# Performance work log

Hardware: AMD Instinct MI355X
Metric: run time of the kernel (lower is better)

Reference implementation:

```python
import jax, jax.numpy as jnp
import numpy as np

EMB_DIM = 512
QKV_DIM = 512
NUM_HEADS = 8
HEAD_DIM = QKV_DIM // NUM_HEADS  # 64
BATCH = 4
SEQLEN = 2048


def _gaussian_orthogonal_random_matrix(rng, nb_rows, nb_cols):
    # Matches torch gaussian_orthogonal_random_matrix with scaling=0.
    blocks = []
    n_full = nb_rows // nb_cols
    for _ in range(n_full):
        q, _ = np.linalg.qr(rng.standard_normal((nb_cols, nb_cols)))
        blocks.append(q.T)
    rem = nb_rows - n_full * nb_cols
    if rem > 0:
        q, _ = np.linalg.qr(rng.standard_normal((nb_cols, nb_cols)))
        blocks.append(q.T[:rem])
    mat = np.concatenate(blocks, axis=0)
    mult = np.linalg.norm(rng.standard_normal((nb_rows, nb_cols)), axis=1)
    return (mult[:, None] * mat).astype(np.float32)


def setup_inputs() -> dict:
    key = jax.random.key(0)
    ks = jax.random.split(key, 9)
    s = 0.02
    inp = {
        'x': jax.random.normal(ks[0], (BATCH, SEQLEN, EMB_DIM), jnp.float32),
        'Wq': jax.random.normal(ks[1], (EMB_DIM, QKV_DIM), jnp.float32) * s,
        'bq': jnp.zeros((QKV_DIM,), jnp.float32),
        'Wk': jax.random.normal(ks[2], (EMB_DIM, QKV_DIM), jnp.float32) * s,
        'bk': jnp.zeros((QKV_DIM,), jnp.float32),
        'Wv': jax.random.normal(ks[3], (EMB_DIM, QKV_DIM), jnp.float32) * s,
        'bv': jnp.zeros((QKV_DIM,), jnp.float32),
        'Wo': jax.random.normal(ks[4], (QKV_DIM, EMB_DIM), jnp.float32) * s,
        'bo': jnp.zeros((EMB_DIM,), jnp.float32),
        'proj': jnp.asarray(_gaussian_orthogonal_random_matrix(
            np.random.default_rng(0), QKV_DIM, HEAD_DIM)),  # (m=qkv_dim, head_dim)
    }
    return inp


def _split_heads(x):
    b, s, _ = x.shape
    return x.reshape(b, s, NUM_HEADS, HEAD_DIM).transpose(0, 2, 1, 3)  # (b,h,s,d)


def _softmax_kernel(data, proj, is_query, eps=1e-4):
    # data: (b,h,n,d); proj: (m,d)
    d = data.shape[-1]
    dn = d ** -0.25                       # data normalizer
    ratio = proj.shape[0] ** -0.5         # m^{-1/2}
    data_dash = jnp.einsum('bhnd,md->bhnm', dn * data, proj)
    diag = jnp.sum(data * data, axis=-1, keepdims=True) * (0.5 * dn * dn)
    if is_query:
        m = jax.lax.stop_gradient(jnp.max(data_dash, axis=-1, keepdims=True))
    else:
        m = jax.lax.stop_gradient(jnp.max(data_dash, axis=(-1, -2), keepdims=True))
    return ratio * (jnp.exp(data_dash - diag - m) + eps)


def _linear_attn(q, k, v):
    # q,k: (b,h,n,m); v: (b,h,n,d)
    k_cumsum = jnp.sum(k, axis=-2)                                  # (b,h,m)
    d_inv = 1.0 / jnp.einsum('bhnm,bhm->bhn', q, k_cumsum)          # (b,h,n)
    context = jnp.einsum('bhnm,bhnd->bhmd', k, v)                   # (b,h,m,d)
    return jnp.einsum('bhmd,bhnm,bhn->bhnd', context, q, d_inv)


def reference(x, Wq, bq, Wk, bk, Wv, bv, Wo, bo, proj):
    q = _split_heads(x @ Wq + bq)
    k = _split_heads(x @ Wk + bk)
    v = _split_heads(x @ Wv + bv)
    qp = _softmax_kernel(q, proj, is_query=True)
    kp = _softmax_kernel(k, proj, is_query=False)
    out = _linear_attn(qp, kp, v)                                   # (b,h,n,d)
    b, h, n, d = out.shape
    out = out.transpose(0, 2, 1, 3).reshape(b, n, h * d)            # combine heads
    return out @ Wo + bo
```

## Files before the change

### kernel.cpp

```cpp
#include <hip/hip_runtime.h>

typedef unsigned short u16;
typedef unsigned int   u32;
typedef __attribute__((ext_vector_type(8))) short bf16x8;
typedef __attribute__((ext_vector_type(4))) short s16x4;
typedef __attribute__((ext_vector_type(4))) float f32x4;

#define MFMA16(a,b,c) __builtin_amdgcn_mfma_f32_16x16x32_bf16((a),(b),(c),0,0,0)

__device__ __forceinline__ float bf2f(u16 u){ return __uint_as_float(((u32)u)<<16); }
__device__ __forceinline__ u16 f2bf(float f){
  u32 u = __float_as_uint(f);
  return (u16)((u + 0x7fffu + ((u>>16)&1u)) >> 16);
}
__device__ __forceinline__ u32 encf(float f){ u32 u=__float_as_uint(f); return (u&0x80000000u)? ~u : (u|0x80000000u); }
__device__ __forceinline__ float decf(u32 u){ return (u&0x80000000u)? __uint_as_float(u&0x7fffffffu) : __uint_as_float(~u); }

__device__ __forceinline__ void async_lds16(u16* lds, const u16* g){
  __builtin_amdgcn_global_load_lds((const __attribute__((address_space(1))) void*)g,
                                   (__attribute__((address_space(3))) void*)lds,
                                   16, 0, 0);
}

template<int ROWS>
__device__ __forceinline__ void stage64(u16* dst, const u16* src, int srcStride, int tid){
  #pragma unroll
  for (int u=tid; u<ROWS*8; u+=256){
    int r=u>>3, c=(u&7)<<3;
    *(int4*)&dst[r*72+c] = *(const int4*)&src[(size_t)r*srcStride + c];
  }
}

__global__ __launch_bounds__(256) void k_setup(u32* kmaxEnc, u16* projS,
    const float* __restrict__ proj, const float* __restrict__ x, u16* __restrict__ xb,
    const float* s0, const float* s1, const float* s2, const float* s3,
    u16* d0, u16* d1, u16* d2, u16* d3)
{
  int bid=blockIdx.x, tid=threadIdx.x;
  if (bid < 1024){
    int z = bid>>8, t = bid&255;
    const float* src = z==0?s0:(z==1?s1:(z==2?s2:s3));
    u16* dst         = z==0?d0:(z==1?d1:(z==2?d2:d3));
    __shared__ u16 tl[32][34];
    int c0=(t&15)*32, r0=(t>>4)*32;
    for (int u=tid; u<1024; u+=256){ int r=u>>5, c=u&31; tl[r][c]=f2bf(src[(size_t)(r0+r)*512 + c0+c]); }
    __syncthreads();
    for (int u=tid; u<1024; u+=256){ int c=u>>5, r=u&31; dst[(size_t)(c0+c)*512 + r0+r]=tl[r][c]; }
  } else {
    int i = (bid-1024)*256 + tid;
    int st = 256*256;
    for (int j=i; j<32; j+=st) kmaxEnc[j]=0u;
    const float dn = 0.35355339059327373f;
    for (int j=i; j<512*64; j+=st) projS[j] = f2bf(dn*proj[j]);
    for (int j=i; j<524288; j+=st){
      float4 a = *(const float4*)&x[(size_t)j*8];
      float4 b = *(const float4*)&x[(size_t)j*8+4];
      u16 tmp[8] = {f2bf(a.x),f2bf(a.y),f2bf(a.z),f2bf(a.w),
                    f2bf(b.x),f2bf(b.y),f2bf(b.z),f2bf(b.w)};
      *(int4*)&xb[(size_t)j*8] = *(const int4*)tmp;
    }
  }
}

__global__ __launch_bounds__(256) void k_prep(const u16* __restrict__ vB, u16* __restrict__ vT,
    float* __restrict__ vsum, const u16* __restrict__ kB, float* __restrict__ diagK)
{
  int bid=blockIdx.x, tid=threadIdx.x;
  if (bid < 4096){
    int xx=bid&1, y=(bid>>1)&63, bh=bid>>7;
    int b=bh>>3, h=bh&7;
    int dd0=xx*32, n0=y*32;
    __shared__ u16 t[32][34];
    const u16* s = vB + (size_t)(b*2048)*512 + h*64;
    for (int u=tid; u<1024; u+=256){ int r=u>>5, c=u&31; t[r][c]=s[(size_t)(n0+r)*512 + dd0+c]; }
    __syncthreads();
    u16* d = vT + (size_t)bh*64*2048;
    for (int u=tid; u<1024; u+=256){ int c=u>>5, r=u&31; d[(size_t)(dd0+c)*2048 + n0+r]=t[r][c]; }
  } else if (bid < 4128){
    int bh=bid-4096; int b=bh>>3, h=bh&7;
    int d=tid&63, part=tid>>6;
    const u16* src = vB + (size_t)(b*2048 + part*512)*512 + h*64 + d;
    float s=0.f;
    for (int n=0;n<512;++n) s += bf2f(src[(size_t)n*512]);
    __shared__ float red[256];
    red[tid]=s; __syncthreads();
    if (part==0) vsum[bh*64+d]=red[d]+red[64+d]+red[128+d]+red[192+d];
  } else {
    int idx=bid-4128;
    int bh=idx&31, seg=idx>>5;
    int b=bh>>3, h=bh&7;
    int part=tid&7;
    const u16* base = kB + (size_t)(b*2048 + seg*256)*512 + h*64 + part*8;
    for (int n0=0; n0<256; n0+=32){
      int n = n0 + (tid>>3);
      bf16x8 v = *(const bf16x8*)&base[(size_t)n*512];
      float sq=0.f;
      #pragma unroll
      for (int j=0;j<8;++j){ float f=bf2f((u16)v[j]); sq+=f*f; }
      sq += __shfl_xor(sq,1,64); sq += __shfl_xor(sq,2,64); sq += __shfl_xor(sq,4,64);
      if (part==0) diagK[(size_t)bh*2048 + seg*256 + n] = 0.0625f*sq;
    }
  }
}

template<bool OF32>
__global__ __launch_bounds__(256) void k_gemm2(const u16* __restrict__ A,
    const u16* BT0, const u16* BT1, const u16* BT2,
    const float* b0, const float* b1, const float* b2,
    void* O0, void* O1, void* O2)
{
  int z = blockIdx.z;
  const u16* BT    = z==0?BT0:(z==1?BT1:BT2);
  const float* bias= z==0?b0 :(z==1?b1 :b2 );
  void* Ov         = z==0?O0 :(z==1?O1 :O2 );
  int bm = blockIdx.x*128, bn = blockIdx.y*64;
  __shared__ u16 sA[128*64];
  __shared__ u16 sB[64*64];
  int tid=threadIdx.x, w=tid>>6, lane=tid&63;
  int lr = lane>>3, lc = (lane&7)*8;
  f32x4 acc[8] = {};
  for (int kk=0; kk<512; kk+=64){
    __syncthreads();
    #pragma unroll
    for (int i=0;i<4;++i){
      int idx = w*4+i;
      async_lds16(&sA[idx*512], A + (size_t)(bm + idx*8 + lr)*512 + kk + lc);
    }
    #pragma unroll
    for (int i=0;i<2;++i){
      int idx = w*2+i;
      async_lds16(&sB[idx*512], BT + (size_t)(bn + idx*8 + lr)*512 + kk + lc);
    }
    __syncthreads();
    int fr = lane&15, kb=(lane>>4)*8;
    #pragma unroll
    for (int rt=0; rt<2; ++rt){
      int ar = (w*2+rt)*16 + fr;
      #pragma unroll
      for (int ct=0; ct<4; ++ct){
        int br = ct*16 + fr;
        #pragma unroll
        for (int kc=0; kc<2; ++kc){
          bf16x8 av = *(const bf16x8*)&sA[ar*64 + kc*32 + kb];
          bf16x8 bv = *(const bf16x8*)&sB[br*64 + kc*32 + kb];
          acc[rt*4+ct] = MFMA16(av,bv,acc[rt*4+ct]);
        }
      }
    }
  }
  int colg = lane&15, rowg=(lane>>4)*4;
  #pragma unroll
  for (int rt=0; rt<2; ++rt){
    #pragma unroll
    for (int ct=0; ct<4; ++ct){
      int col = bn + ct*16 + colg;
      float bv = bias[col];
      #pragma unroll
      for (int j=0;j<4;++j){
        int row = bm + (w*2+rt)*16 + rowg + j;
        if constexpr (OF32) ((float*)Ov)[(size_t)row*512 + col] = acc[rt*4+ct][j] + bv;
        else                ((u16*) Ov)[(size_t)row*512 + col] = f2bf(acc[rt*4+ct][j] + bv);
      }
    }
  }
}

__global__ __launch_bounds__(256) void k_kpctx3(const u16* __restrict__ kB, const u16* __restrict__ projS,
    const u16* __restrict__ vT, const float* __restrict__ diagK,
    float* __restrict__ ctxPT, float* __restrict__ kcsP, u32* __restrict__ kmaxEnc)
{
  int h=blockIdx.x, y=blockIdx.y, b=blockIdx.z;
  int mblk = y&7, s = y>>3;
  int bh=b*8+h;
  int m0 = mblk*64;
  __shared__ __align__(16) u16 sK[128*72];
  __shared__ __align__(16) u16 sV[64*136];
  __shared__ __align__(16) u16 sP[64*72];
  __shared__ __align__(16) u16 sT[64*136];
  __shared__ float sDg[128];
  __shared__ float red[4];
  __shared__ float sRed[4][64];
  int tid=threadIdx.x, w=tid>>6, lane=tid&63;
  int fr=lane&15, kbg=lane>>4, kb=kbg*8, rowg=kbg*4;
  stage64<64>(sP, projS + m0*64, 64, tid);
  f32x4 accc[4]={};
  float sSm[4]={0.f,0.f,0.f,0.f};
  float lm=-3.0e38f;
  const u16* gK = kB + (size_t)(b*2048 + s*1024)*512 + h*64;
  const u16* gV = vT + (size_t)bh*64*2048 + s*1024;
  const float* gD = diagK + (size_t)bh*2048 + s*1024;
  int4 pK[4], pV[4]; float4 pD={0.f,0.f,0.f,0.f};
  #pragma unroll
  for (int i=0;i<4;++i){ int u=tid+i*256; int r=u>>3,c=(u&7)<<3; pK[i]=*(const int4*)&gK[(size_t)r*512 + c]; }
  #pragma unroll
  for (int i=0;i<4;++i){ int u=tid+i*256; int r=u>>4,c=(u&15)<<3; pV[i]=*(const int4*)&gV[(size_t)r*2048 + c]; }
  if (tid<32) pD = *(const float4*)&gD[tid*4];
  for (int nc=0; nc<8; ++nc){
    #pragma unroll
    for (int i=0;i<4;++i){ int u=tid+i*256; int r=u>>3,c=(u&7)<<3; *(int4*)&sK[r*72+c]=pK[i]; }
    #pragma unroll
    for (int i=0;i<4;++i){ int u=tid+i*256; int r=u>>4,c=(u&15)<<3; *(int4*)&sV[r*136+c]=pV[i]; }
    if (tid<32) *(float4*)&sDg[tid*4] = pD;
    __syncthreads();
    if (nc<7){
      #pragma unroll
      for (int i=0;i<4;++i){ int u=tid+i*256; int r=u>>3,c=(u&7)<<3; pK[i]=*(const int4*)&gK[(size_t)((nc+1)*128+r)*512 + c]; }
      #pragma unroll
      for (int i=0;i<4;++i){ int u=tid+i*256; int r=u>>4,c=(u&15)<<3; pV[i]=*(const int4*)&gV[(size_t)r*2048 + (nc+1)*128 + c]; }
      if (tid<32) pD = *(const float4*)&gD[(nc+1)*128 + tid*4];
    }
    f32x4 facc[2][4];
    #pragma unroll
    for (int rt=0;rt<2;++rt){
      int ar=(w*2+rt)*16+fr;
      #pragma unroll
      for (int mt=0;mt<4;++mt){
        f32x4 a={0.f,0.f,0.f,0.f};
        a=MFMA16(*(const bf16x8*)&sK[ar*72+kb],    *(const bf16x8*)&sP[(mt*16+fr)*72+kb],    a);
        a=MFMA16(*(const bf16x8*)&sK[ar*72+32+kb], *(const bf16x8*)&sP[(mt*16+fr)*72+32+kb], a);
        facc[rt][mt]=a;
        lm=fmaxf(lm, fmaxf(fmaxf(a[0],a[1]),fmaxf(a[2],a[3])));
      }
    }
    #pragma unroll
    for (int rt=0;rt<2;++rt){
      int nl=(w*2+rt)*16+rowg;
      #pragma unroll
      for (int mt=0;mt<4;++mt){
        int ml=mt*16+fr;
        s16x4 pk;
        #pragma unroll
        for (int j=0;j<4;++j){
          float vk = __expf(facc[rt][mt][j]-sDg[nl+j]);
          u16 us = f2bf(vk);
          pk[j]=(short)us;
          sSm[mt] += bf2f(us);
        }
        *(s16x4*)&sT[ml*136+nl]=pk;
      }
    }
    __syncthreads();
    int am=w*16+fr;
    #pragma unroll
    for (int ct=0;ct<4;++ct){
      #pragma unroll
      for (int ks=0;ks<4;++ks){
        accc[ct]=MFMA16(*(const bf16x8*)&sT[am*136+ks*32+kb],
                        *(const bf16x8*)&sV[(ct*16+fr)*136+ks*32+kb], accc[ct]);
      }
    }
    __syncthreads();
  }
  #pragma unroll
  for (int mt=0;mt<4;++mt){
    float t=sSm[mt];
    t += __shfl_xor(t,16,64); t += __shfl_xor(t,32,64);
    if (kbg==0) sRed[w][mt*16+fr]=t;
  }
  #pragma unroll
  for (int m2=1;m2<64;m2<<=1) lm=fmaxf(lm,__shfl_xor(lm,m2,64));
  if (lane==0) red[w]=lm;
  float* sTf = (float*)sT;
  int mloc = w*16+rowg;
  #pragma unroll
  for (int ct=0;ct<4;++ct){
    #pragma unroll
    for (int j=0;j<4;++j) sTf[(ct*16+fr)*68 + mloc + j] = accc[ct][j];
  }
  __syncthreads();
  if (tid==0) atomicMax(&kmaxEnc[bh], encf(fmaxf(fmaxf(red[0],red[1]),fmaxf(red[2],red[3]))));
  if (tid<64) kcsP[(size_t)(s*32+bh)*512 + m0 + tid] =
      sRed[0][tid]+sRed[1][tid]+sRed[2][tid]+sRed[3][tid];
  for (int u=tid; u<1024; u+=256){
    int r=u>>4, c=(u&15)*4;
    *(float4*)&ctxPT[((size_t)(s*32+bh)*64 + r)*512 + m0 + c] = *(const float4*)&sTf[r*68+c];
  }
}

__global__ __launch_bounds__(256) void k_comb2(const float* __restrict__ ctxPT, u16* __restrict__ ctxT,
    const float* __restrict__ kcsP, float* __restrict__ kcs,
    float* __restrict__ ctxsum, float* __restrict__ kcssum)
{
  int bh=blockIdx.x, dblk=blockIdx.y;
  int tid=threadIdx.x;
  int d0=dblk*8;
  __shared__ float sDsum[8];
  __shared__ float sKsum[256];
  if (tid<8) sDsum[tid]=0.f;
  __syncthreads();
  const float* p0 = ctxPT + ((size_t)bh*64 + d0)*512;
  const float* p1 = ctxPT + ((size_t)(32+bh)*64 + d0)*512;
  u16* o = ctxT + ((size_t)bh*64 + d0)*512;
  for (int u=tid; u<1024; u+=256){
    int r=u>>7, c=(u&127)*4;
    float4 a=*(const float4*)&p0[(size_t)r*512+c];
    float4 bq=*(const float4*)&p1[(size_t)r*512+c];
    float vx=a.x+bq.x, vy=a.y+bq.y, vz=a.z+bq.z, vw=a.w+bq.w;
    u16 t[4]={f2bf(vx),f2bf(vy),f2bf(vz),f2bf(vw)};
    *(int2*)&o[(size_t)r*512+c] = *(const int2*)t;
    atomicAdd(&sDsum[r], bf2f(t[0])+bf2f(t[1])+bf2f(t[2])+bf2f(t[3]));
  }
  float tpart=0.f;
  if (dblk==0){
    for (int u=tid; u<512; u+=256){
      float t = kcsP[(size_t)bh*512+u] + kcsP[(size_t)(32+bh)*512+u];
      kcs[(size_t)bh*512+u]=t;
      tpart += t;
    }
  }
  sKsum[tid]=tpart;
  __syncthreads();
  if (tid<8) ctxsum[bh*64 + d0 + tid] = sDsum[tid];
  if (dblk==0 && tid<64){
    float a=sKsum[tid]+sKsum[tid+64]+sKsum[tid+128]+sKsum[tid+192];
    #pragma unroll
    for (int m2=1;m2<64;m2<<=1) a += __shfl_xor(a,m2,64);
    if (tid==0) kcssum[bh]=a;
  }
}

__global__ __launch_bounds__(256) void k_qpout2(const u16* __restrict__ qB, const u16* __restrict__ projS,
    const float* __restrict__ kcs, const u16* __restrict__ ctxT,
    const float* __restrict__ ctxsum, const float* __restrict__ kcssum,
    const float* __restrict__ vsum, const u32* __restrict__ kmaxEnc,
    u16* __restrict__ outc)
{
  int h=blockIdx.x, chunk=blockIdx.y, b=blockIdx.z;
  int bh=b*8+h;
  int t0 = b*2048 + chunk*128;
  __shared__ u16 sP[2][64*64];
  __shared__ u16 sCt[2][64*64];
  __shared__ u16 qpL[128*72];
  __shared__ float sK[512];
  __shared__ float diag[128];
  int tid=threadIdx.x, w=tid>>6, lane=tid&63;
  int fr=lane&15, kb=(lane>>4)*8, rowg=(lane>>4)*4;
  bf16x8 qf[2][2];
  #pragma unroll
  for (int rt=0;rt<2;++rt)
    #pragma unroll
    for (int kc=0;kc<2;++kc)
      qf[rt][kc] = *(const bf16x8*)&qB[(size_t)(t0 + w*32 + rt*16 + fr)*512 + h*64 + kc*32 + kb];
  #pragma unroll
  for (int rt=0;rt<2;++rt){
    float s=0.f;
    #pragma unroll
    for (int kc=0;kc<2;++kc)
      #pragma unroll
      for (int j=0;j<8;++j){ float f=bf2f((u16)qf[rt][kc][j]); s+=f*f; }
    s += __shfl_xor(s,16,64); s += __shfl_xor(s,32,64);
    if (lane<16) diag[w*32 + rt*16 + fr] = 0.0625f*s;
  }
  for (int u=tid; u<512; u+=256) sK[u] = kcs[(size_t)bh*512 + u];
  {
    const u16* gp = projS;
    const u16* gc = ctxT + (size_t)bh*64*512;
    int lr=lane>>3, lc=(lane&7)*8;
    #pragma unroll
    for (int i=0;i<2;++i){
      int idx = w*2+i;
      async_lds16(&sP[0][idx*512], gp + idx*512 + lane*8);
      async_lds16(&sCt[0][idx*512], gc + (size_t)(idx*8+lr)*512 + lc);
    }
  }
  f32x4 acc2[2][4]={};
  float mx[2][4], dp[2][4], rs[2][4];
  #pragma unroll
  for (int rt=0;rt<2;++rt)
    #pragma unroll
    for (int j=0;j<4;++j){ mx[rt][j]=-3.0e38f; dp[rt][j]=0.f; rs[rt][j]=0.f; }
  __syncthreads();
  for (int mc=0; mc<8; ++mc){
    int cur = mc&1;
    if (mc<7){
      int nxt = cur^1;
      const u16* gp = projS + (mc+1)*64*64;
      const u16* gc = ctxT + (size_t)bh*64*512 + (mc+1)*64;
      int lr=lane>>3, lc=(lane&7)*8;
      #pragma unroll
      for (int i=0;i<2;++i){
        int idx = w*2+i;
        async_lds16(&sP[nxt][idx*512], gp + idx*512 + lane*8);
        async_lds16(&sCt[nxt][idx*512], gc + (size_t)(idx*8+lr)*512 + lc);
      }
    }
    f32x4 facc[2][4];
    #pragma unroll
    for (int rt=0;rt<2;++rt){
      #pragma unroll
      for (int mt=0;mt<4;++mt){
        f32x4 a={0.f,0.f,0.f,0.f};
        #pragma unroll
        for (int kc=0;kc<2;++kc){
          bf16x8 bv = *(const bf16x8*)&sP[cur][(mt*16+fr)*64 + kc*32 + kb];
          a = MFMA16(qf[rt][kc], bv, a);
        }
        facc[rt][mt]=a;
      }
    }
    #pragma unroll
    for (int rt=0;rt<2;++rt){
      #pragma unroll
      for (int mt=0;mt<4;++mt){
        #pragma unroll
        for (int j=0;j<4;++j){
          int rl = w*32 + rt*16 + rowg + j;
          mx[rt][j] = fmaxf(mx[rt][j], facc[rt][mt][j]);
          float vq = __expf(facc[rt][mt][j] - diag[rl]);
          u16 us = f2bf(vq);
          qpL[rl*72 + mt*16 + fr] = us;
          float uf = bf2f(us);
          dp[rt][j] += uf*sK[mc*64 + mt*16 + fr];
          rs[rt][j] += uf;
        }
      }
    }
    __syncthreads();
    #pragma unroll
    for (int rt=0;rt<2;++rt){
      #pragma unroll
      for (int ct=0;ct<4;++ct){
        #pragma unroll
        for (int kc=0;kc<2;++kc){
          bf16x8 av = *(const bf16x8*)&qpL[(w*32+rt*16+fr)*72 + kc*32 + kb];
          bf16x8 bv = *(const bf16x8*)&sCt[cur][(ct*16+fr)*64 + kc*32 + kb];
          acc2[rt][ct] = MFMA16(av,bv,acc2[rt][ct]);
        }
      }
    }
    __syncthreads();
  }
  #pragma unroll
  for (int rt=0;rt<2;++rt){
    #pragma unroll
    for (int j=0;j<4;++j){
      #pragma unroll
      for (int s=1;s<16;s<<=1){
        dp[rt][j] += __shfl_xor(dp[rt][j],s,64);
        rs[rt][j] += __shfl_xor(rs[rt][j],s,64);
        mx[rt][j]  = fmaxf(mx[rt][j], __shfl_xor(mx[rt][j],s,64));
      }
    }
  }
  float mk  = decf(kmaxEnc[bh]);
  float emk = __expf(mk);
  float Ssum = kcssum[bh];
  const float eps=1e-4f;
  float emq[2][4];
  #pragma unroll
  for (int rt=0;rt<2;++rt)
    #pragma unroll
    for (int j=0;j<4;++j) emq[rt][j]=__expf(mx[rt][j]);
  #pragma unroll
  for (int rt=0;rt<2;++rt){
    #pragma unroll
    for (int ct=0;ct<4;++ct){
      int d = ct*16 + fr;
      float cs = ctxsum[bh*64 + d];
      float vs = vsum[bh*64 + d];
      #pragma unroll
      for (int j=0;j<4;++j){
        float eq = emq[rt][j];
        float numer = acc2[rt][ct][j] + eps*(emk*vs*rs[rt][j] + eq*cs + eps*eq*emk*512.0f*vs);
        float den   = dp[rt][j]       + eps*(emk*2048.0f*rs[rt][j] + eq*Ssum + eps*eq*emk*512.0f*2048.0f);
        int row = t0 + w*32 + rt*16 + rowg + j;
        outc[(size_t)row*512 + h*64 + d] = f2bf(numer/den);
      }
    }
  }
}

extern "C" void kernel_launch(void* const* d_in, const int* in_sizes, int n_in,
                              void* d_out, int out_size, void* d_ws, size_t ws_size,
                              hipStream_t stream)
{
  (void)in_sizes; (void)n_in; (void)out_size; (void)ws_size;
  const float* x    = (const float*)d_in[0];
  const float* Wq   = (const float*)d_in[1];
  const float* bq   = (const float*)d_in[2];
  const float* Wk   = (const float*)d_in[3];
  const float* bk   = (const float*)d_in[4];
  const float* Wv   = (const float*)d_in[5];
  const float* bv   = (const float*)d_in[6];
  const float* Wo   = (const float*)d_in[7];
  const float* bo   = (const float*)d_in[8];
  const float* proj = (const float*)d_in[9];

  char* w = (char*)d_ws;
  size_t off=0;
  auto alloc=[&](size_t bytes)->char*{ char* p=w+off; off=(off+bytes+255)&~(size_t)255; return p; };
  u16*  xb   = (u16*)alloc(8192ull*512*2);
  u16*  qB   = (u16*)alloc(8192ull*512*2);
  u16*  kBf  = (u16*)alloc(8192ull*512*2);
  u16*  vB   = (u16*)alloc(8192ull*512*2);
  u16*  vT   = (u16*)alloc(32ull*64*2048*2);
  u16*  WqT  = (u16*)alloc(512ull*512*2);
  u16*  WkT  = (u16*)alloc(512ull*512*2);
  u16*  WvT  = (u16*)alloc(512ull*512*2);
  u16*  WoT  = (u16*)alloc(512ull*512*2);
  u16*  projS= (u16*)alloc(512ull*64*2);
  u16*  ctxT = (u16*)alloc(32ull*64*512*2);
  float* ctxPT=(float*)alloc(2ull*32*64*512*4);
  float* kcs = (float*)alloc(32ull*512*4);
  float* kcsP= (float*)alloc(2ull*32*512*4);
  float* diagK=(float*)alloc(32ull*2048*4);
  u32*  kmx  = (u32*)alloc(256);
  float* ctxs= (float*)alloc(32ull*64*4);
  float* kcss= (float*)alloc(32ull*4);
  float* vsm = (float*)alloc(32ull*64*4);
  u16*  outc = kBf;

  dim3 TB(256);
  k_setup<<<dim3(1280),TB,0,stream>>>(kmx,projS,proj,x,xb, Wq,Wk,Wv,Wo, WqT,WkT,WvT,WoT);
  k_gemm2<false><<<dim3(64,8,3),TB,0,stream>>>(xb, WqT,WkT,WvT, bq,bk,bv, qB,kBf,vB);
  k_prep<<<dim3(4384),TB,0,stream>>>(vB, vT, vsm, kBf, diagK);
  k_kpctx3<<<dim3(8,16,4),TB,0,stream>>>(kBf, projS, vT, diagK, ctxPT, kcsP, kmx);
  k_comb2<<<dim3(32,8),TB,0,stream>>>(ctxPT, ctxT, kcsP, kcs, ctxs, kcss);
  k_qpout2<<<dim3(8,16,4),TB,0,stream>>>(qB, projS, kcs, ctxT, ctxs, kcss, vsm, kmx, outc);
  k_gemm2<true><<<dim3(64,8,1),TB,0,stream>>>(outc, WoT,WoT,WoT, bo,bo,bo,
                                              d_out,d_out,d_out);
}
```

Measured before the change: 147.2 us.

## Halve q-tile per block, XOR-swizzle LDS tiles, use vmcnt-based soft barriers in qpout

The query-feature/output kernel now processes 64 rows per block instead of 128, doubling the grid to 1024 blocks for better occupancy and latency hiding. Projection and context tiles are loaded with an XOR swizzle to avoid LDS bank conflicts. The context tile is single-buffered and loaded at the start of each step. __syncthreads is replaced with explicit waitcnt+s_barrier so prefetches stay in flight. The cost is twice the projection/context tile loads across blocks and tighter reliance on hand-written wait counts.

```diff
diff --git a/kernel.cpp b/kernel.cpp
--- a/kernel.cpp
+++ b/kernel.cpp
@@ -7,6 +7,11 @@
 typedef __attribute__((ext_vector_type(4))) float f32x4;
 
 #define MFMA16(a,b,c) __builtin_amdgcn_mfma_f32_16x16x32_bf16((a),(b),(c),0,0,0)
+
+#define SOFT_BAR_LG() do{ asm volatile("s_waitcnt lgkmcnt(0)" ::: "memory"); \
+  __builtin_amdgcn_s_barrier(); __builtin_amdgcn_sched_barrier(0); }while(0)
+#define SOFT_BAR_VM(N) do{ asm volatile("s_waitcnt vmcnt(" #N ") lgkmcnt(0)" ::: "memory"); \
+  __builtin_amdgcn_s_barrier(); __builtin_amdgcn_sched_barrier(0); }while(0)
 
 __device__ __forceinline__ float bf2f(u16 u){ return __uint_as_float(((u32)u)<<16); }
 __device__ __forceinline__ u16 f2bf(float f){
@@ -319,7 +324,7 @@
   }
 }
 
-__global__ __launch_bounds__(256) void k_qpout2(const u16* __restrict__ qB, const u16* __restrict__ projS,
+__global__ __launch_bounds__(256) void k_qpout3(const u16* __restrict__ qB, const u16* __restrict__ projS,
     const float* __restrict__ kcs, const u16* __restrict__ ctxT,
     const float* __restrict__ ctxsum, const float* __restrict__ kcssum,
     const float* __restrict__ vsum, const u32* __restrict__ kmaxEnc,
@@ -327,145 +332,121 @@
 {
   int h=blockIdx.x, chunk=blockIdx.y, b=blockIdx.z;
   int bh=b*8+h;
-  int t0 = b*2048 + chunk*128;
+  int t0 = b*2048 + chunk*64;
   __shared__ u16 sP[2][64*64];
-  __shared__ u16 sCt[2][64*64];
-  __shared__ u16 qpL[128*72];
+  __shared__ u16 sCt[64*64];
+  __shared__ u16 qpL[64*72];
   __shared__ float sK[512];
-  __shared__ float diag[128];
+  __shared__ float diag[64];
   int tid=threadIdx.x, w=tid>>6, lane=tid&63;
-  int fr=lane&15, kb=(lane>>4)*8, rowg=(lane>>4)*4;
-  bf16x8 qf[2][2];
-  #pragma unroll
-  for (int rt=0;rt<2;++rt)
+  int fr=lane&15, kbg=lane>>4, kb=kbg*8, rowg=kbg*4;
+  int lr=lane>>3, lgl=((lane&7)^lr)*8;
+  int sw=fr&7;
+  bf16x8 qf[2];
+  #pragma unroll
+  for (int kc=0;kc<2;++kc)
+    qf[kc] = *(const bf16x8*)&qB[(size_t)(t0 + w*16 + fr)*512 + h*64 + kc*32 + kb];
+  {
+    float ssum=0.f;
     #pragma unroll
     for (int kc=0;kc<2;++kc)
-      qf[rt][kc] = *(const bf16x8*)&qB[(size_t)(t0 + w*32 + rt*16 + fr)*512 + h*64 + kc*32 + kb];
-  #pragma unroll
-  for (int rt=0;rt<2;++rt){
-    float s=0.f;
-    #pragma unroll
-    for (int kc=0;kc<2;++kc)
-      #pragma unroll
-      for (int j=0;j<8;++j){ float f=bf2f((u16)qf[rt][kc][j]); s+=f*f; }
-    s += __shfl_xor(s,16,64); s += __shfl_xor(s,32,64);
-    if (lane<16) diag[w*32 + rt*16 + fr] = 0.0625f*s;
+      #pragma unroll
+      for (int j=0;j<8;++j){ float f=bf2f((u16)qf[kc][j]); ssum+=f*f; }
+    ssum += __shfl_xor(ssum,16,64); ssum += __shfl_xor(ssum,32,64);
+    if (lane<16) diag[w*16 + fr] = 0.0625f*ssum;
   }
   for (int u=tid; u<512; u+=256) sK[u] = kcs[(size_t)bh*512 + u];
-  {
-    const u16* gp = projS;
-    const u16* gc = ctxT + (size_t)bh*64*512;
-    int lr=lane>>3, lc=(lane&7)*8;
+  const u16* gcB = ctxT + (size_t)bh*64*512;
+  #pragma unroll
+  for (int i=0;i<2;++i){
+    int idx = w*2+i;
+    async_lds16(&sP[0][idx*512], projS + (size_t)(idx*8+lr)*64 + lgl);
+  }
+  f32x4 acc2[4]={};
+  float mx[4], dp[4], rs[4];
+  #pragma unroll
+  for (int j=0;j<4;++j){ mx[j]=-3.0e38f; dp[j]=0.f; rs[j]=0.f; }
+  SOFT_BAR_VM(0);
+  for (int mc=0; mc<8; ++mc){
+    int cur = mc&1;
     #pragma unroll
     for (int i=0;i<2;++i){
       int idx = w*2+i;
-      async_lds16(&sP[0][idx*512], gp + idx*512 + lane*8);
-      async_lds16(&sCt[0][idx*512], gc + (size_t)(idx*8+lr)*512 + lc);
-    }
-  }
-  f32x4 acc2[2][4]={};
-  float mx[2][4], dp[2][4], rs[2][4];
-  #pragma unroll
-  for (int rt=0;rt<2;++rt)
-    #pragma unroll
-    for (int j=0;j<4;++j){ mx[rt][j]=-3.0e38f; dp[rt][j]=0.f; rs[rt][j]=0.f; }
-  __syncthreads();
-  for (int mc=0; mc<8; ++mc){
-    int cur = mc&1;
+      async_lds16(&sCt[idx*512], gcB + (size_t)(idx*8+lr)*512 + mc*64 + lgl);
+    }
     if (mc<7){
-      int nxt = cur^1;
       const u16* gp = projS + (mc+1)*64*64;
-      const u16* gc = ctxT + (size_t)bh*64*512 + (mc+1)*64;
-      int lr=lane>>3, lc=(lane&7)*8;
       #pragma unroll
       for (int i=0;i<2;++i){
         int idx = w*2+i;
-        async_lds16(&sP[nxt][idx*512], gp + idx*512 + lane*8);
-        async_lds16(&sCt[nxt][idx*512], gc + (size_t)(idx*8+lr)*512 + lc);
-      }
-    }
-    f32x4 facc[2][4];
-    #pragma unroll
-    for (int rt=0;rt<2;++rt){
-      #pragma unroll
-      for (int mt=0;mt<4;++mt){
-        f32x4 a={0.f,0.f,0.f,0.f};
-        #pragma unroll
-        for (int kc=0;kc<2;++kc){
-          bf16x8 bv = *(const bf16x8*)&sP[cur][(mt*16+fr)*64 + kc*32 + kb];
-          a = MFMA16(qf[rt][kc], bv, a);
-        }
-        facc[rt][mt]=a;
-      }
-    }
-    #pragma unroll
-    for (int rt=0;rt<2;++rt){
-      #pragma unroll
-      for (int mt=0;mt<4;++mt){
-        #pragma unroll
-        for (int j=0;j<4;++j){
-          int rl = w*32 + rt*16 + rowg + j;
-          mx[rt][j] = fmaxf(mx[rt][j], facc[rt][mt][j]);
-          float vq = __expf(facc[rt][mt][j] - diag[rl]);
-          u16 us = f2bf(vq);
-          qpL[rl*72 + mt*16 + fr] = us;
-          float uf = bf2f(us);
-          dp[rt][j] += uf*sK[mc*64 + mt*16 + fr];
-          rs[rt][j] += uf;
-        }
-      }
-    }
-    __syncthreads();
-    #pragma unroll
-    for (int rt=0;rt<2;++rt){
-      #pragma unroll
-      for (int ct=0;ct<4;++ct){
-        #pragma unroll
-        for (int kc=0;kc<2;++kc){
-          bf16x8 av = *(const bf16x8*)&qpL[(w*32+rt*16+fr)*72 + kc*32 + kb];
-          bf16x8 bv = *(const bf16x8*)&sCt[cur][(ct*16+fr)*64 + kc*32 + kb];
-          acc2[rt][ct] = MFMA16(av,bv,acc2[rt][ct]);
-        }
-      }
-    }
-    __syncthreads();
-  }
-  #pragma unroll
-  for (int rt=0;rt<2;++rt){
-    #pragma unroll
-    for (int j=0;j<4;++j){
-      #pragma unroll
-      for (int s=1;s<16;s<<=1){
-        dp[rt][j] += __shfl_xor(dp[rt][j],s,64);
-        rs[rt][j] += __shfl_xor(rs[rt][j],s,64);
-        mx[rt][j]  = fmaxf(mx[rt][j], __shfl_xor(mx[rt][j],s,64));
-      }
+        async_lds16(&sP[cur^1][idx*512], gp + (size_t)(idx*8+lr)*64 + lgl);
+      }
+    }
+    f32x4 facc[4];
+    #pragma unroll
+    for (int mt=0;mt<4;++mt){
+      f32x4 a={0.f,0.f,0.f,0.f};
+      #pragma unroll
+      for (int kc=0;kc<2;++kc){
+        bf16x8 bv = *(const bf16x8*)&sP[cur][(mt*16+fr)*64 + (((kc*4+kbg)^sw)<<3)];
+        a = MFMA16(qf[kc], bv, a);
+      }
+      facc[mt]=a;
+    }
+    #pragma unroll
+    for (int mt=0;mt<4;++mt){
+      #pragma unroll
+      for (int j=0;j<4;++j){
+        int rl = w*16 + rowg + j;
+        mx[j] = fmaxf(mx[j], facc[mt][j]);
+        float vq = __expf(facc[mt][j] - diag[rl]);
+        u16 us = f2bf(vq);
+        qpL[rl*72 + mt*16 + fr] = us;
+        float uf = bf2f(us);
+        dp[j] += uf*sK[mc*64 + mt*16 + fr];
+        rs[j] += uf;
+      }
+    }
+    if (mc<7) { SOFT_BAR_VM(2); } else { SOFT_BAR_VM(0); }
+    #pragma unroll
+    for (int ct=0;ct<4;++ct){
+      #pragma unroll
+      for (int kc=0;kc<2;++kc){
+        bf16x8 av = *(const bf16x8*)&qpL[(w*16+fr)*72 + kc*32 + kb];
+        bf16x8 bv = *(const bf16x8*)&sCt[(ct*16+fr)*64 + (((kc*4+kbg)^sw)<<3)];
+        acc2[ct] = MFMA16(av,bv,acc2[ct]);
+      }
+    }
+    if (mc<7) { SOFT_BAR_VM(0); }
+  }
+  #pragma unroll
+  for (int j=0;j<4;++j){
+    #pragma unroll
+    for (int s=1;s<16;s<<=1){
+      dp[j] += __shfl_xor(dp[j],s,64);
+      rs[j] += __shfl_xor(rs[j],s,64);
+      mx[j]  = fmaxf(mx[j], __shfl_xor(mx[j],s,64));
     }
   }
   float mk  = decf(kmaxEnc[bh]);
   float emk = __expf(mk);
   float Ssum = kcssum[bh];
   const float eps=1e-4f;
-  float emq[2][4];
-  #pragma unroll
-  for (int rt=0;rt<2;++rt)
-    #pragma unroll
-    for (int j=0;j<4;++j) emq[rt][j]=__expf(mx[rt][j]);
-  #pragma unroll
-  for (int rt=0;rt<2;++rt){
-    #pragma unroll
-    for (int ct=0;ct<4;++ct){
-      int d = ct*16 + fr;
-      float cs = ctxsum[bh*64 + d];
-      float vs = vsum[bh*64 + d];
-      #pragma unroll
-      for (int j=0;j<4;++j){
-        float eq = emq[rt][j];
-        float numer = acc2[rt][ct][j] + eps*(emk*vs*rs[rt][j] + eq*cs + eps*eq*emk*512.0f*vs);
-        float den   = dp[rt][j]       + eps*(emk*2048.0f*rs[rt][j] + eq*Ssum + eps*eq*emk*512.0f*2048.0f);
-        int row = t0 + w*32 + rt*16 + rowg + j;
-        outc[(size_t)row*512 + h*64 + d] = f2bf(numer/den);
-      }
+  float emq[4];
+  #pragma unroll
+  for (int j=0;j<4;++j) emq[j]=__expf(mx[j]);
+  #pragma unroll
+  for (int ct=0;ct<4;++ct){
+    int d = ct*16 + fr;
+    float cs = ctxsum[bh*64 + d];
+    float vs = vsum[bh*64 + d];
+    #pragma unroll
+    for (int j=0;j<4;++j){
+      float eq = emq[j];
+      float numer = acc2[ct][j] + eps*(emk*vs*rs[j] + eq*cs + eps*eq*emk*512.0f*vs);
+      float den   = dp[j]       + eps*(emk*2048.0f*rs[j] + eq*Ssum + eps*eq*emk*512.0f*2048.0f);
+      int row = t0 + w*16 + rowg + j;
+      outc[(size_t)row*512 + h*64 + d] = f2bf(numer/den);
     }
   }
 }
@@ -516,7 +497,7 @@
   k_prep<<<dim3(4384),TB,0,stream>>>(vB, vT, vsm, kBf, diagK);
   k_kpctx3<<<dim3(8,16,4),TB,0,stream>>>(kBf, projS, vT, diagK, ctxPT, kcsP, kmx);
   k_comb2<<<dim3(32,8),TB,0,stream>>>(ctxPT, ctxT, kcsP, kcs, ctxs, kcss);
-  k_qpout2<<<dim3(8,16,4),TB,0,stream>>>(qB, projS, kcs, ctxT, ctxs, kcss, vsm, kmx, outc);
+  k_qpout3<<<dim3(8,32,4),TB,0,stream>>>(qB, projS, kcs, ctxT, ctxs, kcss, vsm, kmx, outc);
   k_gemm2<true><<<dim3(64,8,1),TB,0,stream>>>(outc, WoT,WoT,WoT, bo,bo,bo,
                                               d_out,d_out,d_out);
 }
```

Result: no change. 145.0 us (-1.5%).
